# Kernel tuning notes

Hardware: AMD Instinct MI355X
Metric: run time of the kernel (lower is better)

Reference implementation:

```python
import jax, jax.numpy as jnp
import numpy as np

IN_F = 4096
OUT_F = 4096
BATCH = 4096


def _dequantize(q, mn, mx):
    # Faithful to dequantize_to_float32: per-tensor affine using the *observed*
    # integer min/max of the stored tensor.
    q_min = q.min()
    q_max = q.max()
    scale = (mx - mn) / (q_max - q_min).astype(jnp.float32)
    return (q - q_min).astype(jnp.float32) * scale + mn


def setup_inputs() -> dict:
    key = jax.random.key(0)
    k1, k2, k3 = jax.random.split(key, 3)
    x = jax.random.normal(k1, (BATCH, IN_F), dtype=jnp.float32)
    # int8-valued weights/bias stored as int32 (same math; dequant uses tensor min/max)
    weight_q = jax.random.randint(k2, (OUT_F, IN_F), -128, 128, dtype=jnp.int32)
    bias_q = jax.random.randint(k3, (OUT_F,), -128, 128, dtype=jnp.int32)
    # per-tensor float range recorded at quantization time (original scales by 255 first,
    # so these ranges are on the scaled tensor; any floats work for correctness testing)
    weight_min = jnp.float32(-4.2)
    weight_max = jnp.float32(4.5)
    bias_min = jnp.float32(-1.3)
    bias_max = jnp.float32(1.1)
    return {
        "x": x,
        "weight_q": weight_q,
        "bias_q": bias_q,
        "weight_min": weight_min,
        "weight_max": weight_max,
        "bias_min": bias_min,
        "bias_max": bias_max,
    }


def reference(x, weight_q, bias_q, weight_min, weight_max, bias_min, bias_max):
    w = _dequantize(weight_q, weight_min, weight_max)   # [OUT_F, IN_F] fp32
    b = _dequantize(bias_q, bias_min, bias_max)         # [OUT_F] fp32
    # F.linear: x @ W^T + b
    return jnp.einsum("bi,oi->bo", x, w) + b
```

## Files before the change

### kernel.cpp

```cpp
#include <hip/hip_runtime.h>
#include <climits>

#define IN_F 4096
#define OUT_F 4096
#define BATCH 4096
#define NPART 1024

typedef __bf16 bf16x8 __attribute__((ext_vector_type(8)));
typedef float f32x4 __attribute__((ext_vector_type(4)));

__device__ __forceinline__ unsigned short f2bf_rne(float f) {
  unsigned int u = __float_as_uint(f);
  u += 0x7fffu + ((u >> 16) & 1u);
  return (unsigned short)(u >> 16);
}

__global__ __launch_bounds__(256) void k_conv(const float* __restrict__ x,
                                              const int* __restrict__ q,
                                              unsigned short* __restrict__ xb,
                                              unsigned short* __restrict__ qb,
                                              float* __restrict__ rowsum,
                                              int* __restrict__ pmin,
                                              int* __restrict__ pmax) {
  if (blockIdx.x < NPART) {
    const int n4 = (OUT_F * IN_F) / 4;
    const int stride = NPART * 256;
    int vmin = INT_MAX, vmax = INT_MIN;
    const int4* q4 = (const int4*)q;
    ushort4* qb4 = (ushort4*)qb;
    for (int i = blockIdx.x * 256 + threadIdx.x; i < n4; i += stride) {
      int4 v = q4[i];
      vmin = min(vmin, min(min(v.x, v.y), min(v.z, v.w)));
      vmax = max(vmax, max(max(v.x, v.y), max(v.z, v.w)));
      ushort4 h;
      h.x = f2bf_rne((float)v.x);
      h.y = f2bf_rne((float)v.y);
      h.z = f2bf_rne((float)v.z);
      h.w = f2bf_rne((float)v.w);
      qb4[i] = h;
    }
    for (int off = 32; off > 0; off >>= 1) {
      vmin = min(vmin, __shfl_down(vmin, off));
      vmax = max(vmax, __shfl_down(vmax, off));
    }
    __shared__ int rmin[4], rmax[4];
    const int wave = threadIdx.x >> 6;
    if ((threadIdx.x & 63) == 0) { rmin[wave] = vmin; rmax[wave] = vmax; }
    __syncthreads();
    if (threadIdx.x == 0) {
      pmin[blockIdx.x] = min(min(rmin[0], rmin[1]), min(rmin[2], rmin[3]));
      pmax[blockIdx.x] = max(max(rmax[0], rmax[1]), max(rmax[2], rmax[3]));
    }
  } else {
    const int wave = threadIdx.x >> 6;
    const int lane = threadIdx.x & 63;
    const int row = (blockIdx.x - NPART) * 4 + wave;
    const float4* xr = (const float4*)(x + (size_t)row * IN_F);
    ushort4* xbr = (ushort4*)(xb + (size_t)row * IN_F);
    float s = 0.f;
#pragma unroll
    for (int it = 0; it < IN_F / 4 / 64; ++it) {
      const int i = it * 64 + lane;
      float4 v = xr[i];
      s += (v.x + v.y) + (v.z + v.w);
      ushort4 h;
      h.x = f2bf_rne(v.x); h.y = f2bf_rne(v.y);
      h.z = f2bf_rne(v.z); h.w = f2bf_rne(v.w);
      xbr[i] = h;
    }
    for (int off = 32; off > 0; off >>= 1) s += __shfl_down(s, off);
    if (lane == 0) rowsum[row] = s;
  }
}

__global__ __launch_bounds__(256) void k_wmm(const int* __restrict__ q,
                                             int* __restrict__ pmin,
                                             int* __restrict__ pmax) {
  const int n4 = (OUT_F * IN_F) / 4;
  const int stride = gridDim.x * blockDim.x;
  int vmin = INT_MAX, vmax = INT_MIN;
  const int4* q4 = (const int4*)q;
  for (int i = blockIdx.x * blockDim.x + threadIdx.x; i < n4; i += stride) {
    int4 v = q4[i];
    vmin = min(vmin, min(min(v.x, v.y), min(v.z, v.w)));
    vmax = max(vmax, max(max(v.x, v.y), max(v.z, v.w)));
  }
  for (int off = 32; off > 0; off >>= 1) {
    vmin = min(vmin, __shfl_down(vmin, off));
    vmax = max(vmax, __shfl_down(vmax, off));
  }
  __shared__ int rmin[4], rmax[4];
  const int wave = threadIdx.x >> 6;
  if ((threadIdx.x & 63) == 0) { rmin[wave] = vmin; rmax[wave] = vmax; }
  __syncthreads();
  if (threadIdx.x == 0) {
    pmin[blockIdx.x] = min(min(rmin[0], rmin[1]), min(rmin[2], rmin[3]));
    pmax[blockIdx.x] = max(max(rmax[0], rmax[1]), max(rmax[2], rmax[3]));
  }
}

__global__ __launch_bounds__(256) void k_scal(const int* __restrict__ pmin,
                                              const int* __restrict__ pmax, int npart,
                                              const int* __restrict__ bq,
                                              const float* __restrict__ wmn,
                                              const float* __restrict__ wmx,
                                              const float* __restrict__ bmn,
                                              const float* __restrict__ bmx,
                                              float* __restrict__ scal) {
  int vmin = INT_MAX, vmax = INT_MIN;
  for (int i = threadIdx.x; i < npart; i += 256) {
    vmin = min(vmin, pmin[i]);
    vmax = max(vmax, pmax[i]);
  }
  int bmin = INT_MAX, bmaxv = INT_MIN;
  for (int i = threadIdx.x; i < OUT_F; i += 256) {
    int v = bq[i];
    bmin = min(bmin, v);
    bmaxv = max(bmaxv, v);
  }
  for (int off = 32; off > 0; off >>= 1) {
    vmin = min(vmin, __shfl_down(vmin, off));
    vmax = max(vmax, __shfl_down(vmax, off));
    bmin = min(bmin, __shfl_down(bmin, off));
    bmaxv = max(bmaxv, __shfl_down(bmaxv, off));
  }
  __shared__ int r[4][4];
  const int wave = threadIdx.x >> 6;
  if ((threadIdx.x & 63) == 0) {
    r[wave][0] = vmin; r[wave][1] = vmax; r[wave][2] = bmin; r[wave][3] = bmaxv;
  }
  __syncthreads();
  if (threadIdx.x == 0) {
    int qmin = min(min(r[0][0], r[1][0]), min(r[2][0], r[3][0]));
    int qmax = max(max(r[0][1], r[1][1]), max(r[2][1], r[3][1]));
    int qbmin = min(min(r[0][2], r[1][2]), min(r[2][2], r[3][2]));
    int qbmax = max(max(r[0][3], r[1][3]), max(r[2][3], r[3][3]));
    float ws = (*wmx - *wmn) / (float)(qmax - qmin);
    scal[0] = ws;
    scal[1] = *wmn - ws * (float)qmin;
    float bs = (*bmx - *bmn) / (float)(qbmax - qbmin);
    scal[2] = bs;
    scal[3] = *bmn - bs * (float)qbmin;
  }
}

__device__ __forceinline__ void load_lds16(const unsigned short* g, unsigned short* l) {
  __builtin_amdgcn_global_load_lds(
      (const __attribute__((address_space(1))) unsigned int*)g,
      (__attribute__((address_space(3))) unsigned int*)l, 16, 0, 0);
}

__global__ __launch_bounds__(512, 2) void k_gemm(
    const unsigned short* __restrict__ A,
    const unsigned short* __restrict__ B,
    const int* __restrict__ bq,
    const float* __restrict__ rowsum,
    const float* __restrict__ scal,
    float* __restrict__ C) {
  __shared__ __align__(16) unsigned short As[4][8192];
  __shared__ __align__(16) unsigned short Bs[4][8192];

  const int tid = threadIdx.x;
  const int w = tid >> 6;
  const int lane = tid & 63;
  const int bm = blockIdx.x * 256;
  const int bn = blockIdx.y * 256;

  const int wm = (w & 1) * 128;
  const int wn = (w >> 1) * 64;
  const int r16 = lane & 15;
  const int q = lane >> 4;
  const int pc = (q ^ ((r16 >> 1) & 3)) * 8;

  const int cA0 = w * 128 + lane;
  const int rowS0 = cA0 >> 2;
  const int colS0 = ((cA0 & 3) ^ ((rowS0 >> 1) & 3)) * 8;
  const int cA1 = cA0 + 64;
  const int rowS1 = cA1 >> 2;
  const int colS1 = ((cA1 & 3) ^ ((rowS1 >> 1) & 3)) * 8;
  const unsigned short* srcA0 = A + (size_t)(bm + rowS0) * IN_F + colS0;
  const unsigned short* srcA1 = A + (size_t)(bm + rowS1) * IN_F + colS1;
  const unsigned short* srcB0 = B + (size_t)(bn + rowS0) * IN_F + colS0;
  const unsigned short* srcB1 = B + (size_t)(bn + rowS1) * IN_F + colS1;
  const int dst0 = w * 1024;
  const int dst1 = w * 1024 + 512;

  f32x4 acc[8][4] = {};

  const int NT = IN_F / 32;

#pragma unroll
  for (int t = 0; t < 3; ++t) {
    load_lds16(srcA0 + t * 32, &As[t][dst0]);
    load_lds16(srcA1 + t * 32, &As[t][dst1]);
    load_lds16(srcB0 + t * 32, &Bs[t][dst0]);
    load_lds16(srcB1 + t * 32, &Bs[t][dst1]);
  }
  asm volatile("s_waitcnt vmcnt(8)" ::: "memory");
  __builtin_amdgcn_s_barrier();

  for (int t = 0; t < NT; ++t) {
    const int s = t & 3;
    const unsigned short* Asl = As[s];
    const unsigned short* Bsl = Bs[s];
    const int s3 = (t + 3) & 3;
    const int koff = (t + 3) * 32;
    const bool pf = (t + 3 < NT);

    bf16x8 afr[4], bfr[4];
#pragma unroll
    for (int i = 0; i < 4; ++i)
      afr[i] = *(const bf16x8*)&Asl[(wm + i * 16 + r16) * 32 + pc];
#pragma unroll
    for (int i = 0; i < 4; ++i)
      bfr[i] = *(const bf16x8*)&Bsl[(wn + i * 16 + r16) * 32 + pc];
    if (pf) {
      load_lds16(srcA0 + koff, &As[s3][dst0]);
      load_lds16(srcA1 + koff, &As[s3][dst1]);
    }
    __builtin_amdgcn_s_barrier();
    __builtin_amdgcn_s_setprio(1);
#pragma unroll
    for (int mi = 0; mi < 4; ++mi)
#pragma unroll
      for (int ni = 0; ni < 4; ++ni)
        acc[mi][ni] = __builtin_amdgcn_mfma_f32_16x16x32_bf16(afr[mi], bfr[ni], acc[mi][ni], 0, 0, 0);
    __builtin_amdgcn_s_setprio(0);
    __builtin_amdgcn_s_barrier();

    bf16x8 af2[4];
#pragma unroll
    for (int i = 0; i < 4; ++i)
      af2[i] = *(const bf16x8*)&Asl[(wm + 64 + i * 16 + r16) * 32 + pc];
    if (pf) {
      load_lds16(srcB0 + koff, &Bs[s3][dst0]);
      load_lds16(srcB1 + koff, &Bs[s3][dst1]);
    }
    __builtin_amdgcn_s_barrier();
    __builtin_amdgcn_s_setprio(1);
#pragma unroll
    for (int mi = 0; mi < 4; ++mi)
#pragma unroll
      for (int ni = 0; ni < 4; ++ni)
        acc[4 + mi][ni] = __builtin_amdgcn_mfma_f32_16x16x32_bf16(af2[mi], bfr[ni], acc[4 + mi][ni], 0, 0, 0);
    __builtin_amdgcn_s_setprio(0);

    if (t < NT - 3)       asm volatile("s_waitcnt vmcnt(8)" ::: "memory");
    else if (t == NT - 3) asm volatile("s_waitcnt vmcnt(4)" ::: "memory");
    else if (t == NT - 2) asm volatile("s_waitcnt vmcnt(0)" ::: "memory");
    __builtin_amdgcn_s_barrier();
  }

  const float wsc = scal[0], wbe = scal[1], bsc = scal[2], bbe = scal[3];
#pragma unroll
  for (int ni = 0; ni < 4; ++ni) {
    const int gn = bn + wn + ni * 16 + r16;
    const float bdq = bsc * (float)bq[gn] + bbe;
#pragma unroll
    for (int mi = 0; mi < 8; ++mi) {
      const int gm0 = bm + wm + mi * 16 + q * 4;
#pragma unroll
      for (int r = 0; r < 4; ++r) {
        const int gm = gm0 + r;
        C[(size_t)gm * OUT_F + gn] = wsc * acc[mi][ni][r] + wbe * rowsum[gm] + bdq;
      }
    }
  }
}

__global__ void k_naive(const float* __restrict__ x, const int* __restrict__ wq,
                        const int* __restrict__ bq, const float* __restrict__ scal,
                        float* __restrict__ out) {
  const int o = blockIdx.x * blockDim.x + threadIdx.x;
  const int b = blockIdx.y;
  const float* xr = x + (size_t)b * IN_F;
  const int* wr = wq + (size_t)o * IN_F;
  float s = 0.f, sx = 0.f;
  for (int k = 0; k < IN_F; ++k) {
    float xv = xr[k];
    s += xv * (float)wr[k];
    sx += xv;
  }
  out[(size_t)b * OUT_F + o] =
      scal[0] * s + scal[1] * sx + scal[2] * (float)bq[o] + scal[3];
}

extern "C" void kernel_launch(void* const* d_in, const int* in_sizes, int n_in,
                              void* d_out, int out_size, void* d_ws, size_t ws_size,
                              hipStream_t stream) {
  const float* x = (const float*)d_in[0];
  const int* wq = (const int*)d_in[1];
  const int* bq = (const int*)d_in[2];
  const float* wmn = (const float*)d_in[3];
  const float* wmx = (const float*)d_in[4];
  const float* bmn = (const float*)d_in[5];
  const float* bmx = (const float*)d_in[6];
  float* out = (float*)d_out;

  char* ws = (char*)d_ws;
  float* scal = (float*)ws;
  int* pmin = (int*)(ws + 64);
  int* pmax = (int*)(ws + 64 + NPART * 4);
  float* rowsum = (float*)(ws + 64 + 2 * NPART * 4);
  unsigned short* xb = (unsigned short*)(ws + 32768);
  unsigned short* qb = xb + (size_t)BATCH * IN_F;
  const size_t needed = 32768 + (size_t)BATCH * IN_F * 2 + (size_t)OUT_F * IN_F * 2;

  if (ws_size >= needed) {
    k_conv<<<2 * NPART, 256, 0, stream>>>(x, wq, xb, qb, rowsum, pmin, pmax);
    k_scal<<<1, 256, 0, stream>>>(pmin, pmax, NPART, bq, wmn, wmx, bmn, bmx, scal);
    dim3 grid(BATCH / 256, OUT_F / 256);
    k_gemm<<<grid, 512, 0, stream>>>(xb, qb, bq, rowsum, scal, out);
  } else {
    k_wmm<<<NPART, 256, 0, stream>>>(wq, pmin, pmax);
    k_scal<<<1, 256, 0, stream>>>(pmin, pmax, NPART, bq, wmn, wmx, bmn, bmx, scal);
    k_naive<<<dim3(OUT_F / 256, BATCH), 256, 0, stream>>>(x, wq, bq, scal, out);
  }
}
```

Baseline: 318.8 us.

## Register double-buffer GEMM fragments and cut to one barrier per k-step

The main GEMM loop is rewritten as a macro unrolled by the four LDS stages. The A/B fragments for the next k-step are now loaded into a second register set while the current step's MFMAs run. This removes two of the three workgroup barriers per iteration and lets LDS reads overlap matrix math. The vmcnt waits are retuned so the stage needed next has landed before each barrier. The cost is extra VGPRs for the second fragment set and a longer explicit tail sequence, which may raise register pressure at two waves per SIMD.

```diff
diff --git a/kernel.cpp b/kernel.cpp
--- a/kernel.cpp
+++ b/kernel.cpp
@@ -150,6 +150,45 @@
       (__attribute__((address_space(3))) unsigned int*)l, 16, 0, 0);
 }
 
+#define VMW(n) asm volatile("s_waitcnt vmcnt(" #n ")" ::: "memory")
+#define CFENCE asm volatile("" ::: "memory")
+
+#define GITER(C, CA, CB, NA, NB, PF, LDN, CHK)                                      \
+  {                                                                                 \
+    bf16x8 a2_[4];                                                                  \
+    _Pragma("unroll") for (int i = 0; i < 4; ++i)                                   \
+        a2_[i] = *(const bf16x8*)&As[(C)][(wm + 64 + i * 16 + r16) * 32 + pc];      \
+    if (PF) {                                                                       \
+      load_lds16(srcA0 + kb + ((C) + 3) * 32, &As[((C) + 3) & 3][dst0]);            \
+      load_lds16(srcA1 + kb + ((C) + 3) * 32, &As[((C) + 3) & 3][dst1]);            \
+    }                                                                               \
+    __builtin_amdgcn_s_setprio(1);                                                  \
+    _Pragma("unroll") for (int mi = 0; mi < 4; ++mi)                                \
+        _Pragma("unroll") for (int ni = 0; ni < 4; ++ni)                            \
+            acc[mi][ni] = __builtin_amdgcn_mfma_f32_16x16x32_bf16(                  \
+                CA[mi], CB[ni], acc[mi][ni], 0, 0, 0);                              \
+    __builtin_amdgcn_s_setprio(0);                                                  \
+    if (LDN) {                                                                      \
+      _Pragma("unroll") for (int i = 0; i < 4; ++i) {                               \
+        NA[i] = *(const bf16x8*)&As[((C) + 1) & 3][(wm + i * 16 + r16) * 32 + pc];  \
+        NB[i] = *(const bf16x8*)&Bs[((C) + 1) & 3][(wn + i * 16 + r16) * 32 + pc];  \
+      }                                                                             \
+    }                                                                               \
+    if (PF) {                                                                       \
+      load_lds16(srcB0 + kb + ((C) + 3) * 32, &Bs[((C) + 3) & 3][dst0]);            \
+      load_lds16(srcB1 + kb + ((C) + 3) * 32, &Bs[((C) + 3) & 3][dst1]);            \
+    }                                                                               \
+    __builtin_amdgcn_s_setprio(1);                                                  \
+    _Pragma("unroll") for (int mi = 0; mi < 4; ++mi)                                \
+        _Pragma("unroll") for (int ni = 0; ni < 4; ++ni)                            \
+            acc[4 + mi][ni] = __builtin_amdgcn_mfma_f32_16x16x32_bf16(              \
+                a2_[mi], CB[ni], acc[4 + mi][ni], 0, 0, 0);                         \
+    __builtin_amdgcn_s_setprio(0);                                                  \
+    CHK;                                                                            \
+    __builtin_amdgcn_s_barrier();                                                   \
+    CFENCE;                                                                         \
+  }
+
 __global__ __launch_bounds__(512, 2) void k_gemm(
     const unsigned short* __restrict__ A,
     const unsigned short* __restrict__ B,
@@ -186,8 +225,7 @@
   const int dst1 = w * 1024 + 512;
 
   f32x4 acc[8][4] = {};
-
-  const int NT = IN_F / 32;
+  bf16x8 fa0[4], fb0[4], fa1[4], fb1[4];
 
 #pragma unroll
   for (int t = 0; t < 3; ++t) {
@@ -196,59 +234,28 @@
     load_lds16(srcB0 + t * 32, &Bs[t][dst0]);
     load_lds16(srcB1 + t * 32, &Bs[t][dst1]);
   }
-  asm volatile("s_waitcnt vmcnt(8)" ::: "memory");
+  VMW(4);
   __builtin_amdgcn_s_barrier();
-
-  for (int t = 0; t < NT; ++t) {
-    const int s = t & 3;
-    const unsigned short* Asl = As[s];
-    const unsigned short* Bsl = Bs[s];
-    const int s3 = (t + 3) & 3;
-    const int koff = (t + 3) * 32;
-    const bool pf = (t + 3 < NT);
-
-    bf16x8 afr[4], bfr[4];
-#pragma unroll
-    for (int i = 0; i < 4; ++i)
-      afr[i] = *(const bf16x8*)&Asl[(wm + i * 16 + r16) * 32 + pc];
-#pragma unroll
-    for (int i = 0; i < 4; ++i)
-      bfr[i] = *(const bf16x8*)&Bsl[(wn + i * 16 + r16) * 32 + pc];
-    if (pf) {
-      load_lds16(srcA0 + koff, &As[s3][dst0]);
-      load_lds16(srcA1 + koff, &As[s3][dst1]);
-    }
-    __builtin_amdgcn_s_barrier();
-    __builtin_amdgcn_s_setprio(1);
-#pragma unroll
-    for (int mi = 0; mi < 4; ++mi)
-#pragma unroll
-      for (int ni = 0; ni < 4; ++ni)
-        acc[mi][ni] = __builtin_amdgcn_mfma_f32_16x16x32_bf16(afr[mi], bfr[ni], acc[mi][ni], 0, 0, 0);
-    __builtin_amdgcn_s_setprio(0);
-    __builtin_amdgcn_s_barrier();
-
-    bf16x8 af2[4];
-#pragma unroll
-    for (int i = 0; i < 4; ++i)
-      af2[i] = *(const bf16x8*)&Asl[(wm + 64 + i * 16 + r16) * 32 + pc];
-    if (pf) {
-      load_lds16(srcB0 + koff, &Bs[s3][dst0]);
-      load_lds16(srcB1 + koff, &Bs[s3][dst1]);
-    }
-    __builtin_amdgcn_s_barrier();
-    __builtin_amdgcn_s_setprio(1);
-#pragma unroll
-    for (int mi = 0; mi < 4; ++mi)
-#pragma unroll
-      for (int ni = 0; ni < 4; ++ni)
-        acc[4 + mi][ni] = __builtin_amdgcn_mfma_f32_16x16x32_bf16(af2[mi], bfr[ni], acc[4 + mi][ni], 0, 0, 0);
-    __builtin_amdgcn_s_setprio(0);
-
-    if (t < NT - 3)       asm volatile("s_waitcnt vmcnt(8)" ::: "memory");
-    else if (t == NT - 3) asm volatile("s_waitcnt vmcnt(4)" ::: "memory");
-    else if (t == NT - 2) asm volatile("s_waitcnt vmcnt(0)" ::: "memory");
-    __builtin_amdgcn_s_barrier();
+  CFENCE;
+#pragma unroll
+  for (int i = 0; i < 4; ++i) {
+    fa0[i] = *(const bf16x8*)&As[0][(wm + i * 16 + r16) * 32 + pc];
+    fb0[i] = *(const bf16x8*)&Bs[0][(wn + i * 16 + r16) * 32 + pc];
+  }
+
+  for (int u = 0; u < 31; ++u) {
+    const int kb = u * 128;
+    GITER(0, fa0, fb0, fa1, fb1, 1, 1, VMW(4));
+    GITER(1, fa1, fb1, fa0, fb0, 1, 1, VMW(4));
+    GITER(2, fa0, fb0, fa1, fb1, 1, 1, VMW(4));
+    GITER(3, fa1, fb1, fa0, fb0, 1, 1, VMW(4));
+  }
+  {
+    const int kb = 31 * 128;
+    GITER(0, fa0, fb0, fa1, fb1, 1, 1, VMW(4));
+    GITER(1, fa1, fb1, fa0, fb0, 0, 1, VMW(0));
+    GITER(2, fa0, fb0, fa1, fb1, 0, 1, ((void)0));
+    GITER(3, fa1, fb1, fa0, fb0, 0, 0, ((void)0));
   }
 
   const float wsc = scal[0], wbe = scal[1], bsc = scal[2], bbe = scal[3];
```

New measurement: 314.4 us. No clear change (-1.4%).

## Fuse bf16 conversion and scale computation into GEMM main loop

Applied to the files above, without the earlier changes.

Removes the separate conversion pass that wrote bf16 copies of x and the weights to workspace. The GEMM now loads fp32 x and int32 weights straight from global memory, converts them to bf16 in registers and writes them to a double-buffered LDS tile. The row sums are accumulated during the main loop, and each block recomputes the dequant scales from the per-partition min/max, so the k_scal launch also goes away. The cost is that every GEMM block reads data at twice the width (fp32/int32 instead of bf16) and repeats that read across output tiles. The async global-to-LDS 4-stage pipeline is replaced by a register-staged 2-stage one with full __syncthreads each step, which may expose memory latency.

```diff
diff --git a/kernel.cpp b/kernel.cpp
--- a/kernel.cpp
+++ b/kernel.cpp
@@ -8,6 +8,7 @@
 
 typedef __bf16 bf16x8 __attribute__((ext_vector_type(8)));
 typedef float f32x4 __attribute__((ext_vector_type(4)));
+typedef unsigned short u16x8 __attribute__((ext_vector_type(8)));
 
 __device__ __forceinline__ unsigned short f2bf_rne(float f) {
   unsigned int u = __float_as_uint(f);
@@ -15,62 +16,19 @@
   return (unsigned short)(u >> 16);
 }
 
-__global__ __launch_bounds__(256) void k_conv(const float* __restrict__ x,
-                                              const int* __restrict__ q,
-                                              unsigned short* __restrict__ xb,
-                                              unsigned short* __restrict__ qb,
-                                              float* __restrict__ rowsum,
-                                              int* __restrict__ pmin,
-                                              int* __restrict__ pmax) {
-  if (blockIdx.x < NPART) {
-    const int n4 = (OUT_F * IN_F) / 4;
-    const int stride = NPART * 256;
-    int vmin = INT_MAX, vmax = INT_MIN;
-    const int4* q4 = (const int4*)q;
-    ushort4* qb4 = (ushort4*)qb;
-    for (int i = blockIdx.x * 256 + threadIdx.x; i < n4; i += stride) {
-      int4 v = q4[i];
-      vmin = min(vmin, min(min(v.x, v.y), min(v.z, v.w)));
-      vmax = max(vmax, max(max(v.x, v.y), max(v.z, v.w)));
-      ushort4 h;
-      h.x = f2bf_rne((float)v.x);
-      h.y = f2bf_rne((float)v.y);
-      h.z = f2bf_rne((float)v.z);
-      h.w = f2bf_rne((float)v.w);
-      qb4[i] = h;
-    }
-    for (int off = 32; off > 0; off >>= 1) {
-      vmin = min(vmin, __shfl_down(vmin, off));
-      vmax = max(vmax, __shfl_down(vmax, off));
-    }
-    __shared__ int rmin[4], rmax[4];
-    const int wave = threadIdx.x >> 6;
-    if ((threadIdx.x & 63) == 0) { rmin[wave] = vmin; rmax[wave] = vmax; }
-    __syncthreads();
-    if (threadIdx.x == 0) {
-      pmin[blockIdx.x] = min(min(rmin[0], rmin[1]), min(rmin[2], rmin[3]));
-      pmax[blockIdx.x] = max(max(rmax[0], rmax[1]), max(rmax[2], rmax[3]));
-    }
-  } else {
-    const int wave = threadIdx.x >> 6;
-    const int lane = threadIdx.x & 63;
-    const int row = (blockIdx.x - NPART) * 4 + wave;
-    const float4* xr = (const float4*)(x + (size_t)row * IN_F);
-    ushort4* xbr = (ushort4*)(xb + (size_t)row * IN_F);
-    float s = 0.f;
-#pragma unroll
-    for (int it = 0; it < IN_F / 4 / 64; ++it) {
-      const int i = it * 64 + lane;
-      float4 v = xr[i];
-      s += (v.x + v.y) + (v.z + v.w);
-      ushort4 h;
-      h.x = f2bf_rne(v.x); h.y = f2bf_rne(v.y);
-      h.z = f2bf_rne(v.z); h.w = f2bf_rne(v.w);
-      xbr[i] = h;
-    }
-    for (int off = 32; off > 0; off >>= 1) s += __shfl_down(s, off);
-    if (lane == 0) rowsum[row] = s;
-  }
+__device__ __forceinline__ u16x8 cvt8f(float4 a, float4 b) {
+  u16x8 h;
+  h[0] = f2bf_rne(a.x); h[1] = f2bf_rne(a.y); h[2] = f2bf_rne(a.z); h[3] = f2bf_rne(a.w);
+  h[4] = f2bf_rne(b.x); h[5] = f2bf_rne(b.y); h[6] = f2bf_rne(b.z); h[7] = f2bf_rne(b.w);
+  return h;
+}
+__device__ __forceinline__ u16x8 cvt8i(int4 a, int4 b) {
+  u16x8 h;
+  h[0] = f2bf_rne((float)a.x); h[1] = f2bf_rne((float)a.y);
+  h[2] = f2bf_rne((float)a.z); h[3] = f2bf_rne((float)a.w);
+  h[4] = f2bf_rne((float)b.x); h[5] = f2bf_rne((float)b.y);
+  h[6] = f2bf_rne((float)b.z); h[7] = f2bf_rne((float)b.w);
+  return h;
 }
 
 __global__ __launch_bounds__(256) void k_wmm(const int* __restrict__ q,
@@ -144,21 +102,22 @@
   }
 }
 
-__device__ __forceinline__ void load_lds16(const unsigned short* g, unsigned short* l) {
-  __builtin_amdgcn_global_load_lds(
-      (const __attribute__((address_space(1))) unsigned int*)g,
-      (__attribute__((address_space(3))) unsigned int*)l, 16, 0, 0);
-}
+#define CFENCE asm volatile("" ::: "memory")
 
 __global__ __launch_bounds__(512, 2) void k_gemm(
-    const unsigned short* __restrict__ A,
-    const unsigned short* __restrict__ B,
+    const float* __restrict__ X,
+    const int* __restrict__ WQ,
     const int* __restrict__ bq,
-    const float* __restrict__ rowsum,
-    const float* __restrict__ scal,
+    const int* __restrict__ pmin,
+    const int* __restrict__ pmax,
+    const float* __restrict__ wmn, const float* __restrict__ wmx,
+    const float* __restrict__ bmn, const float* __restrict__ bmx,
     float* __restrict__ C) {
-  __shared__ __align__(16) unsigned short As[4][8192];
-  __shared__ __align__(16) unsigned short Bs[4][8192];
+  __shared__ __align__(16) unsigned short As[2][8192];
+  __shared__ __align__(16) unsigned short Bs[2][8192];
+  __shared__ float rowsumS[256];
+  __shared__ int rr[8][4];
+  __shared__ float s_scal[4];
 
   const int tid = threadIdx.x;
   const int w = tid >> 6;
@@ -166,6 +125,41 @@
   const int bm = blockIdx.x * 256;
   const int bn = blockIdx.y * 256;
 
+  {
+    int vmin = INT_MAX, vmax = INT_MIN;
+    for (int i = tid; i < NPART; i += 512) {
+      vmin = min(vmin, pmin[i]);
+      vmax = max(vmax, pmax[i]);
+    }
+    int bmn_ = INT_MAX, bmx_ = INT_MIN;
+    for (int i = tid; i < OUT_F; i += 512) {
+      int v = bq[i];
+      bmn_ = min(bmn_, v);
+      bmx_ = max(bmx_, v);
+    }
+    for (int off = 32; off > 0; off >>= 1) {
+      vmin = min(vmin, __shfl_down(vmin, off));
+      vmax = max(vmax, __shfl_down(vmax, off));
+      bmn_ = min(bmn_, __shfl_down(bmn_, off));
+      bmx_ = max(bmx_, __shfl_down(bmx_, off));
+    }
+    if ((tid & 63) == 0) { rr[w][0] = vmin; rr[w][1] = vmax; rr[w][2] = bmn_; rr[w][3] = bmx_; }
+    __syncthreads();
+    if (tid == 0) {
+      int qmin = rr[0][0], qmax = rr[0][1], qbmin = rr[0][2], qbmax = rr[0][3];
+      for (int i = 1; i < 8; ++i) {
+        qmin = min(qmin, rr[i][0]); qmax = max(qmax, rr[i][1]);
+        qbmin = min(qbmin, rr[i][2]); qbmax = max(qbmax, rr[i][3]);
+      }
+      float ws = (*wmx - *wmn) / (float)(qmax - qmin);
+      s_scal[0] = ws;
+      s_scal[1] = *wmn - ws * (float)qmin;
+      float bs = (*bmx - *bmn) / (float)(qbmax - qbmin);
+      s_scal[2] = bs;
+      s_scal[3] = *bmn - bs * (float)qbmin;
+    }
+  }
+
   const int wm = (w & 1) * 128;
   const int wn = (w >> 1) * 64;
   const int r16 = lane & 15;
@@ -175,94 +169,119 @@
   const int cA0 = w * 128 + lane;
   const int rowS0 = cA0 >> 2;
   const int colS0 = ((cA0 & 3) ^ ((rowS0 >> 1) & 3)) * 8;
-  const int cA1 = cA0 + 64;
-  const int rowS1 = cA1 >> 2;
-  const int colS1 = ((cA1 & 3) ^ ((rowS1 >> 1) & 3)) * 8;
-  const unsigned short* srcA0 = A + (size_t)(bm + rowS0) * IN_F + colS0;
-  const unsigned short* srcA1 = A + (size_t)(bm + rowS1) * IN_F + colS1;
-  const unsigned short* srcB0 = B + (size_t)(bn + rowS0) * IN_F + colS0;
-  const unsigned short* srcB1 = B + (size_t)(bn + rowS1) * IN_F + colS1;
-  const int dst0 = w * 1024;
-  const int dst1 = w * 1024 + 512;
+  const int rowS1 = rowS0 + 16;
+  const int colS1 = ((cA0 & 3) ^ ((rowS1 >> 1) & 3)) * 8;
+  const float* xs0 = X + (size_t)(bm + rowS0) * IN_F + colS0;
+  const float* xs1 = X + (size_t)(bm + rowS1) * IN_F + colS1;
+  const int* ws0 = WQ + (size_t)(bn + rowS0) * IN_F + colS0;
+  const int* ws1 = WQ + (size_t)(bn + rowS1) * IN_F + colS1;
+  const int dstu0 = w * 1024 + lane * 8;
+  const int dstu1 = dstu0 + 512;
 
   f32x4 acc[8][4] = {};
+  float rsum0 = 0.f, rsum1 = 0.f;
 
   const int NT = IN_F / 32;
 
-#pragma unroll
-  for (int t = 0; t < 3; ++t) {
-    load_lds16(srcA0 + t * 32, &As[t][dst0]);
-    load_lds16(srcA1 + t * 32, &As[t][dst1]);
-    load_lds16(srcB0 + t * 32, &Bs[t][dst0]);
-    load_lds16(srcB1 + t * 32, &Bs[t][dst1]);
-  }
-  asm volatile("s_waitcnt vmcnt(8)" ::: "memory");
-  __builtin_amdgcn_s_barrier();
+  {
+    float4 a0a = *(const float4*)(xs0);
+    float4 a0b = *(const float4*)(xs0 + 4);
+    float4 a1a = *(const float4*)(xs1);
+    float4 a1b = *(const float4*)(xs1 + 4);
+    int4 b0a = *(const int4*)(ws0);
+    int4 b0b = *(const int4*)(ws0 + 4);
+    int4 b1a = *(const int4*)(ws1);
+    int4 b1b = *(const int4*)(ws1 + 4);
+    rsum0 += ((a0a.x + a0a.y) + (a0a.z + a0a.w)) + ((a0b.x + a0b.y) + (a0b.z + a0b.w));
+    rsum1 += ((a1a.x + a1a.y) + (a1a.z + a1a.w)) + ((a1b.x + a1b.y) + (a1b.z + a1b.w));
+    *(u16x8*)&As[0][dstu0] = cvt8f(a0a, a0b);
+    *(u16x8*)&As[0][dstu1] = cvt8f(a1a, a1b);
+    *(u16x8*)&Bs[0][dstu0] = cvt8i(b0a, b0b);
+    *(u16x8*)&Bs[0][dstu1] = cvt8i(b1a, b1b);
+  }
+  __syncthreads();
 
   for (int t = 0; t < NT; ++t) {
-    const int s = t & 3;
+    const int s = t & 1;
+    const int d = s ^ 1;
     const unsigned short* Asl = As[s];
     const unsigned short* Bsl = Bs[s];
-    const int s3 = (t + 3) & 3;
-    const int koff = (t + 3) * 32;
-    const bool pf = (t + 3 < NT);
-
-    bf16x8 afr[4], bfr[4];
+    const int koff = (t + 1) * 32;
+    const bool pf = (t + 1 < NT);
+
+    float4 a0a, a0b, a1a, a1b;
+    int4 b0a, b0b, b1a, b1b;
+    if (pf) {
+      a0a = *(const float4*)(xs0 + koff);
+      a0b = *(const float4*)(xs0 + koff + 4);
+      a1a = *(const float4*)(xs1 + koff);
+      a1b = *(const float4*)(xs1 + koff + 4);
+      b0a = *(const int4*)(ws0 + koff);
+      b0b = *(const int4*)(ws0 + koff + 4);
+      b1a = *(const int4*)(ws1 + koff);
+      b1b = *(const int4*)(ws1 + koff + 4);
+    }
+    CFENCE;
+
+    bf16x8 fa[4], fb[4];
 #pragma unroll
     for (int i = 0; i < 4; ++i)
-      afr[i] = *(const bf16x8*)&Asl[(wm + i * 16 + r16) * 32 + pc];
+      fa[i] = *(const bf16x8*)&Asl[(wm + i * 16 + r16) * 32 + pc];
 #pragma unroll
     for (int i = 0; i < 4; ++i)
-      bfr[i] = *(const bf16x8*)&Bsl[(wn + i * 16 + r16) * 32 + pc];
+      fb[i] = *(const bf16x8*)&Bsl[(wn + i * 16 + r16) * 32 + pc];
+    __builtin_amdgcn_s_setprio(1);
+#pragma unroll
+    for (int mi = 0; mi < 4; ++mi)
+#pragma unroll
+      for (int ni = 0; ni < 4; ++ni)
+        acc[mi][ni] = __builtin_amdgcn_mfma_f32_16x16x32_bf16(fa[mi], fb[ni], acc[mi][ni], 0, 0, 0);
+    __builtin_amdgcn_s_setprio(0);
+    bf16x8 fa2[4];
+#pragma unroll
+    for (int i = 0; i < 4; ++i)
+      fa2[i] = *(const bf16x8*)&Asl[(wm + 64 + i * 16 + r16) * 32 + pc];
+    __builtin_amdgcn_s_setprio(1);
+#pragma unroll
+    for (int mi = 0; mi < 4; ++mi)
+#pragma unroll
+      for (int ni = 0; ni < 4; ++ni)
+        acc[4 + mi][ni] = __builtin_amdgcn_mfma_f32_16x16x32_bf16(fa2[mi], fb[ni], acc[4 + mi][ni], 0, 0, 0);
+    __builtin_amdgcn_s_setprio(0);
+
     if (pf) {
-      load_lds16(srcA0 + koff, &As[s3][dst0]);
-      load_lds16(srcA1 + koff, &As[s3][dst1]);
-    }
-    __builtin_amdgcn_s_barrier();
-    __builtin_amdgcn_s_setprio(1);
-#pragma unroll
-    for (int mi = 0; mi < 4; ++mi)
-#pragma unroll
-      for (int ni = 0; ni < 4; ++ni)
-        acc[mi][ni] = __builtin_amdgcn_mfma_f32_16x16x32_bf16(afr[mi], bfr[ni], acc[mi][ni], 0, 0, 0);
-    __builtin_amdgcn_s_setprio(0);
-    __builtin_amdgcn_s_barrier();
-
-    bf16x8 af2[4];
-#pragma unroll
-    for (int i = 0; i < 4; ++i)
-      af2[i] = *(const bf16x8*)&Asl[(wm + 64 + i * 16 + r16) * 32 + pc];
-    if (pf) {
-      load_lds16(srcB0 + koff, &Bs[s3][dst0]);
-      load_lds16(srcB1 + koff, &Bs[s3][dst1]);
-    }
-    __builtin_amdgcn_s_barrier();
-    __builtin_amdgcn_s_setprio(1);
-#pragma unroll
-    for (int mi = 0; mi < 4; ++mi)
-#pragma unroll
-      for (int ni = 0; ni < 4; ++ni)
-        acc[4 + mi][ni] = __builtin_amdgcn_mfma_f32_16x16x32_bf16(af2[mi], bfr[ni], acc[4 + mi][ni], 0, 0, 0);
-    __builtin_amdgcn_s_setprio(0);
-
-    if (t < NT - 3)       asm volatile("s_waitcnt vmcnt(8)" ::: "memory");
-    else if (t == NT - 3) asm volatile("s_waitcnt vmcnt(4)" ::: "memory");
-    else if (t == NT - 2) asm volatile("s_waitcnt vmcnt(0)" ::: "memory");
-    __builtin_amdgcn_s_barrier();
-  }
-
-  const float wsc = scal[0], wbe = scal[1], bsc = scal[2], bbe = scal[3];
+      rsum0 += ((a0a.x + a0a.y) + (a0a.z + a0a.w)) + ((a0b.x + a0b.y) + (a0b.z + a0b.w));
+      rsum1 += ((a1a.x + a1a.y) + (a1a.z + a1a.w)) + ((a1b.x + a1b.y) + (a1b.z + a1b.w));
+      *(u16x8*)&As[d][dstu0] = cvt8f(a0a, a0b);
+      *(u16x8*)&As[d][dstu1] = cvt8f(a1a, a1b);
+      *(u16x8*)&Bs[d][dstu0] = cvt8i(b0a, b0b);
+      *(u16x8*)&Bs[d][dstu1] = cvt8i(b1a, b1b);
+    }
+    __syncthreads();
+  }
+
+  rsum0 += __shfl_down(rsum0, 2);
+  rsum0 += __shfl_down(rsum0, 1);
+  rsum1 += __shfl_down(rsum1, 2);
+  rsum1 += __shfl_down(rsum1, 1);
+  if ((lane & 3) == 0) {
+    rowsumS[rowS0] = rsum0;
+    rowsumS[rowS1] = rsum1;
+  }
+  __syncthreads();
+
+  const float wsc = s_scal[0], wbe = s_scal[1], bsc = s_scal[2], bbe = s_scal[3];
 #pragma unroll
   for (int ni = 0; ni < 4; ++ni) {
     const int gn = bn + wn + ni * 16 + r16;
     const float bdq = bsc * (float)bq[gn] + bbe;
 #pragma unroll
     for (int mi = 0; mi < 8; ++mi) {
-      const int gm0 = bm + wm + mi * 16 + q * 4;
+      const int lm0 = wm + mi * 16 + q * 4;
 #pragma unroll
       for (int r = 0; r < 4; ++r) {
-        const int gm = gm0 + r;
-        C[(size_t)gm * OUT_F + gn] = wsc * acc[mi][ni][r] + wbe * rowsum[gm] + bdq;
+        const int lm = lm0 + r;
+        C[(size_t)(bm + lm) * OUT_F + gn] = wsc * acc[mi][ni][r] + wbe * rowsumS[lm] + bdq;
       }
     }
   }
@@ -301,16 +320,13 @@
   float* scal = (float*)ws;
   int* pmin = (int*)(ws + 64);
   int* pmax = (int*)(ws + 64 + NPART * 4);
-  float* rowsum = (float*)(ws + 64 + 2 * NPART * 4);
-  unsigned short* xb = (unsigned short*)(ws + 32768);
-  unsigned short* qb = xb + (size_t)BATCH * IN_F;
-  const size_t needed = 32768 + (size_t)BATCH * IN_F * 2 + (size_t)OUT_F * IN_F * 2;
+  const size_t needed = 64 + 2 * NPART * 4;
 
   if (ws_size >= needed) {
-    k_conv<<<2 * NPART, 256, 0, stream>>>(x, wq, xb, qb, rowsum, pmin, pmax);
-    k_scal<<<1, 256, 0, stream>>>(pmin, pmax, NPART, bq, wmn, wmx, bmn, bmx, scal);
+    k_wmm<<<NPART, 256, 0, stream>>>(wq, pmin, pmax);
     dim3 grid(BATCH / 256, OUT_F / 256);
-    k_gemm<<<grid, 512, 0, stream>>>(xb, qb, bq, rowsum, scal, out);
+    k_gemm<<<grid, 512, 0, stream>>>(x, wq, bq, pmin, pmax,
+                                     wmn, wmx, bmn, bmx, out);
   } else {
     k_wmm<<<NPART, 256, 0, stream>>>(wq, pmin, pmax);
     k_scal<<<1, 256, 0, stream>>>(pmin, pmax, NPART, bq, wmn, wmx, bmn, bmx, scal);
```

After: 420.8 us. 32.0% more time.
